# Optimization experiments

Measured on AMD Instinct MI355X. Metric: run time of the kernel, lower is better.

## Reference

```python
import jax, jax.numpy as jnp
import numpy as np

B, H, W, C = 2, 64, 64, 192
DM = int(2.0 * C)   # d_inner = ssm_ratio * hidden_dim = 384
N = 16              # d_state
R = 12              # dt_rank = ceil(C / 16)
K = 4               # scan directions


def _ln(x, g, b, eps):
    mu = jnp.mean(x, axis=-1, keepdims=True)
    var = jnp.var(x, axis=-1, keepdims=True)
    return (x - mu) * jax.lax.rsqrt(var + eps) * g + b


def setup_inputs() -> dict:
    key = jax.random.key(0)
    ks = jax.random.split(key, 8)
    return {
        "input": jax.random.normal(ks[0], (B, H, W, C), jnp.float32),
        "norm_g": jnp.ones((C,), jnp.float32),
        "norm_b": jnp.zeros((C,), jnp.float32),
        "in_proj_w": jax.random.normal(ks[1], (C, 2 * DM), jnp.float32) * 0.02,
        "conv_w": jax.random.normal(ks[2], (DM, 1, 3, 3), jnp.float32) * 0.1,
        "conv_b": jnp.zeros((DM,), jnp.float32),
        "x_proj_w": jax.random.normal(ks[3], (K, R + 2 * N, DM), jnp.float32) * 0.02,
        "dt_w": jax.random.normal(ks[4], (K, DM, R), jnp.float32) * 0.1,
        "dt_b": jax.random.uniform(ks[5], (K, DM), jnp.float32, -4.0, -2.0),
        "A_logs": jnp.tile(jnp.log(jnp.arange(1, N + 1, dtype=jnp.float32))[None, None, :], (K, DM, 1)),
        "Ds": jnp.ones((K, DM), jnp.float32),
        "out_norm_g": jnp.ones((DM,), jnp.float32),
        "out_norm_b": jnp.zeros((DM,), jnp.float32),
        "out_proj_w": jax.random.normal(ks[6], (DM, C), jnp.float32) * 0.02,
    }


def _selective_scan(us, deltas, A, Bs, Cs):
    # us, deltas: (B,K,D,L); A: (K,D,N); Bs, Cs: (B,K,N,L)
    u_l = jnp.moveaxis(us, -1, 0)       # (L,B,K,D)
    d_l = jnp.moveaxis(deltas, -1, 0)   # (L,B,K,D)
    B_l = jnp.moveaxis(Bs, -1, 0)       # (L,B,K,N)
    C_l = jnp.moveaxis(Cs, -1, 0)       # (L,B,K,N)
    h0 = jnp.zeros(us.shape[:3] + (A.shape[-1],), us.dtype)  # (B,K,D,N)

    def step(h, xs):
        u_t, d_t, b_t, c_t = xs
        dA = jnp.exp(d_t[..., None] * A)                       # (B,K,D,N)
        h = dA * h + (d_t * u_t)[..., None] * b_t[:, :, None, :]
        y = jnp.einsum('bkdn,bkn->bkd', h, c_t)
        return h, y

    _, ys = jax.lax.scan(step, h0, (u_l, d_l, B_l, C_l))
    return jnp.moveaxis(ys, 0, -1)  # (B,K,D,L)


def reference(input, norm_g, norm_b, in_proj_w, conv_w, conv_b, x_proj_w,
              dt_w, dt_b, A_logs, Ds, out_norm_g, out_norm_b, out_proj_w):
    Bz, Hh, Ww, Cc = input.shape
    L = Hh * Ww
    # pre-norm
    xn = _ln(input, norm_g, norm_b, 1e-6)
    # input projection -> x, z
    xz = xn @ in_proj_w                      # (B,H,W,2*DM)
    x, z = jnp.split(xz, 2, axis=-1)
    # depthwise conv + SiLU (channels-first)
    x = jnp.transpose(x, (0, 3, 1, 2))       # (B,DM,H,W)
    Dm = x.shape[1]
    x = jax.lax.conv_general_dilated(
        x, conv_w, (1, 1), 'SAME',
        dimension_numbers=('NCHW', 'OIHW', 'NCHW'),
        feature_group_count=Dm) + conv_b[None, :, None, None]
    x = jax.nn.silu(x)
    # 4-direction cross-scan: hw, wh, and their reverses
    x_flat = x.reshape(Bz, Dm, L)
    x_t = jnp.transpose(x, (0, 1, 3, 2)).reshape(Bz, Dm, L)
    xs = jnp.stack([x_flat, x_t], axis=1)                  # (B,2,DM,L)
    xs = jnp.concatenate([xs, jnp.flip(xs, -1)], axis=1)   # (B,4,DM,L)
    Rr = dt_w.shape[2]
    Nn = A_logs.shape[2]
    x_dbl = jnp.einsum('bkdl,kcd->bkcl', xs, x_proj_w)     # (B,4,R+2N,L)
    dts, Bs, Cs = jnp.split(x_dbl, [Rr, Rr + Nn], axis=2)
    deltas = jax.nn.softplus(
        jnp.einsum('bkrl,kdr->bkdl', dts, dt_w) + dt_b[None, :, :, None])
    A = -jnp.exp(A_logs)                                   # (4,DM,N)
    out_y = _selective_scan(xs, deltas, A, Bs, Cs) + Ds[None, :, :, None] * xs
    # merge the 4 directions back
    inv = jnp.flip(out_y[:, 2:], -1)

    def wh(t):
        return jnp.transpose(t.reshape(Bz, Dm, Ww, Hh), (0, 1, 3, 2)).reshape(Bz, Dm, L)

    y = out_y[:, 0] + inv[:, 0] + wh(out_y[:, 1]) + wh(inv[:, 1])  # (B,DM,L)
    y = jnp.transpose(y, (0, 2, 1))                                # (B,L,DM)
    y = _ln(y, out_norm_g, out_norm_b, 1e-5).reshape(Bz, Hh, Ww, Dm)
    y = y * jax.nn.silu(z)
    out = y @ out_proj_w
    # residual (drop_path=0 -> identity)
    return input + out
```

## Files before the change

kernel.cpp:

```cpp
#include <hip/hip_runtime.h>
#include <hip/hip_bf16.h>


typedef __attribute__((ext_vector_type(8))) short short8;
typedef __attribute__((ext_vector_type(4))) float floatx4;

__global__ __launch_bounds__(256) void k_ln(const float* __restrict__ in,
                                            const float* __restrict__ g,
                                            const float* __restrict__ be,
                                            __hip_bfloat16* __restrict__ out) {
  int row = blockIdx.x * 4 + (threadIdx.x >> 6);
  int lane = threadIdx.x & 63;
  const float* x = in + (long)row * 192;
  float v0 = x[lane], v1 = x[lane + 64], v2 = x[lane + 128];
  float s = v0 + v1 + v2;
  float s2 = v0 * v0 + v1 * v1 + v2 * v2;
  #pragma unroll
  for (int o = 32; o > 0; o >>= 1) { s += __shfl_xor(s, o); s2 += __shfl_xor(s2, o); }
  float mu = s * (1.f / 192.f);
  float var = s2 * (1.f / 192.f) - mu * mu;
  float r = rsqrtf(var + 1e-6f);
  __hip_bfloat16* op = out + (long)row * 192;
  op[lane]       = __float2bfloat16((v0 - mu) * r * g[lane]       + be[lane]);
  op[lane + 64]  = __float2bfloat16((v1 - mu) * r * g[lane + 64]  + be[lane + 64]);
  op[lane + 128] = __float2bfloat16((v2 - mu) * r * g[lane + 128] + be[lane + 128]);
}

__global__ __launch_bounds__(256) void k_packw(const float* __restrict__ ipw,
                                               const float* __restrict__ xpw,
                                               const float* __restrict__ opw,
                                               __hip_bfloat16* __restrict__ Wt1,
                                               __hip_bfloat16* __restrict__ Wt2,
                                               __hip_bfloat16* __restrict__ Wt3) {
  int idx = blockIdx.x * 256 + threadIdx.x;
  if (idx < 147456) {
    int n = idx / 192, k = idx - n * 192;
    Wt1[idx] = __float2bfloat16(ipw[(long)k * 768 + n]);
  } else if (idx < 147456 + 73728) {
    int t = idx - 147456;
    int j = t / 384;
    float v = (j < 176) ? xpw[t] : 0.f;
    Wt2[t] = __float2bfloat16(v);
  } else if (idx < 147456 + 73728 + 73728) {
    int t = idx - 147456 - 73728;
    int n = t / 384, k = t - n * 384;
    Wt3[t] = __float2bfloat16(opw[(long)k * 192 + n]);
  }
}

__device__ __forceinline__ int inv_dir(int k, int p) {
  int pt = ((p & 63) << 6) | (p >> 6);
  if (k == 0) return p;
  if (k == 1) return pt;
  if (k == 2) return 4095 - p;
  return 4095 - pt;
}
__device__ __forceinline__ int dir_pix(int k, int l) { return inv_dir(k, l); }

template <int EPI>
__global__ __launch_bounds__(256) void k_gemm_mfma(const __hip_bfloat16* __restrict__ A,
                                                   const __hip_bfloat16* __restrict__ Bt,
                                                   const float* __restrict__ Res,
                                                   float* __restrict__ Co,
                                                   __hip_bfloat16* __restrict__ CoB,
                                                   __hip_bfloat16* __restrict__ Co2B,
                                                   float* __restrict__ dtsS,
                                                   float* __restrict__ BsS,
                                                   float* __restrict__ CsS,
                                                   int M, int N, int Kk) {
  __shared__ __align__(16) short As[64 * 64];
  __shared__ __align__(16) short Bs[64 * 64];
  int tid = threadIdx.x;
  int wave = tid >> 6, lane = tid & 63;
  int mlane = lane & 15, quad = lane >> 4;
  int row0 = blockIdx.y * 64, col0 = blockIdx.x * 64;
  int wr = wave & 1, wc = wave >> 1;
  floatx4 acc[2][2];
  #pragma unroll
  for (int mi = 0; mi < 2; mi++)
    #pragma unroll
    for (int ni = 0; ni < 2; ni++) acc[mi][ni] = (floatx4){0.f, 0.f, 0.f, 0.f};

  for (int k0 = 0; k0 < Kk; k0 += 64) {
    #pragma unroll
    for (int c = tid; c < 512; c += 256) {
      int r = c >> 3, j = c & 7;
      *(float4*)&As[r * 64 + ((j ^ (r & 7)) << 3)] =
          *(const float4*)&A[(long)(row0 + r) * Kk + k0 + j * 8];
    }
    #pragma unroll
    for (int c = tid; c < 512; c += 256) {
      int r = c >> 3, j = c & 7;
      *(float4*)&Bs[r * 64 + ((j ^ (r & 7)) << 3)] =
          *(const float4*)&Bt[(long)(col0 + r) * Kk + k0 + j * 8];
    }
    __syncthreads();
    short8 af[2][2], bf[2][2];
    #pragma unroll
    for (int mi = 0; mi < 2; mi++) {
      int r = wr * 32 + mi * 16 + mlane;
      #pragma unroll
      for (int kk = 0; kk < 2; kk++) {
        int jx = (kk * 4 + quad) ^ (r & 7);
        af[mi][kk] = *(const short8*)&As[r * 64 + jx * 8];
      }
    }
    #pragma unroll
    for (int ni = 0; ni < 2; ni++) {
      int rn = wc * 32 + ni * 16 + mlane;
      #pragma unroll
      for (int kk = 0; kk < 2; kk++) {
        int jx = (kk * 4 + quad) ^ (rn & 7);
        bf[ni][kk] = *(const short8*)&Bs[rn * 64 + jx * 8];
      }
    }
    #pragma unroll
    for (int kk = 0; kk < 2; kk++)
      #pragma unroll
      for (int mi = 0; mi < 2; mi++)
        #pragma unroll
        for (int ni = 0; ni < 2; ni++)
          acc[mi][ni] = __builtin_amdgcn_mfma_f32_16x16x32_bf16(af[mi][kk], bf[ni][kk],
                                                                acc[mi][ni], 0, 0, 0);
    __syncthreads();
  }
  #pragma unroll
  for (int mi = 0; mi < 2; mi++) {
    #pragma unroll
    for (int ni = 0; ni < 2; ni++) {
      int cc = col0 + wc * 32 + ni * 16 + mlane;
      #pragma unroll
      for (int i = 0; i < 4; i++) {
        int rr = row0 + wr * 32 + mi * 16 + quad * 4 + i;
        float v = acc[mi][ni][i];
        if (EPI == 1) {
          Co[(long)rr * N + cc] = v + Res[(long)rr * N + cc];
        } else if (EPI == 2) {
          if (cc < 384) CoB[(long)rr * 384 + cc] = __float2bfloat16(v);
          else          Co2B[(long)rr * 384 + (cc - 384)] = __float2bfloat16(v);
        } else {
          if (cc < 176) {
            int k4 = (cc >= 132) ? 3 : (cc >= 88) ? 2 : (cc >= 44) ? 1 : 0;
            int c = cc - k4 * 44;
            int b = rr >> 12, p = rr & 4095;
            long lbase = ((long)((b << 2) + k4) << 12) + p;
            if (c < 12)      dtsS[lbase * 12 + c] = v;
            else if (c < 28) BsS[lbase * 16 + (c - 12)] = v;
            else             CsS[lbase * 16 + (c - 28)] = v;
          }
        }
      }
    }
  }
}

__global__ __launch_bounds__(384) void k_conv(const __hip_bfloat16* __restrict__ xbufB,
                                              const float* __restrict__ cw,
                                              const float* __restrict__ cb,
                                              __hip_bfloat16* __restrict__ xcb) {
  int row = blockIdx.x;
  int b = row >> 12, p = row & 4095;
  int h = p >> 6, w0 = p & 63;
  int d = threadIdx.x;
  float acc = cb[d];
  const float* wt = cw + d * 9;
  #pragma unroll
  for (int dh = -1; dh <= 1; dh++) {
    int hh = h + dh;
    if (hh < 0 || hh > 63) continue;
    #pragma unroll
    for (int dw = -1; dw <= 1; dw++) {
      int ww = w0 + dw;
      if (ww < 0 || ww > 63) continue;
      acc += __bfloat162float(xbufB[((long)(b << 12) + (hh << 6) + ww) * 384 + d])
             * wt[(dh + 1) * 3 + (dw + 1)];
    }
  }
  float sg = 1.f / (1.f + __expf(-acc));
  xcb[(long)row * 384 + d] = __float2bfloat16(acc * sg);
}

__device__ __forceinline__ void pow16(float r, float* pws) {
  pws[0] = r;
  #pragma unroll
  for (int n = 1; n < 16; n++) {
    int m = n + 1, c = (m + 1) / 2, f = m - c;
    pws[n] = pws[c - 1] * pws[f - 1];
  }
}

__global__ __launch_bounds__(384) void k_scan0(
    const float* __restrict__ dtsS, const float* __restrict__ BsS,
    const __hip_bfloat16* __restrict__ xcb,
    const float* __restrict__ A_logs, const float* __restrict__ dt_w,
    const float* __restrict__ dt_b,
    float* __restrict__ Eb, float* __restrict__ Dend) {
  int bid = blockIdx.x;
  int s = bid & 127, bk = bid >> 7;
  int k = bk & 3, b = bk >> 2;
  int d = threadIdx.x;
  float w[12];
  const float* dwp = dt_w + ((long)(k * 384) + d) * 12;
  #pragma unroll
  for (int r = 0; r < 12; r++) w[r] = dwp[r];
  float db = dt_b[k * 384 + d];
  const float* al = A_logs + ((long)(k * 384) + d) * 16;
  bool pw = true;
  float av[16];
  #pragma unroll
  for (int n = 0; n < 16; n++) {
    float a = __expf(al[n]);
    av[n] = -a;
    pw = pw && (fabsf(a - (float)(n + 1)) < 1e-3f);
  }
  float h[16];
  #pragma unroll
  for (int n = 0; n < 16; n++) h[n] = 0.f;
  float cum = 0.f;
  long bpk = (long)bk << 12;
  long bpix = (long)(b << 12);

  if (pw) {
    #pragma unroll 4
    for (int t = 0; t < 32; t++) {
      int p = dir_pix(k, s * 32 + t);
      const float4* dq = (const float4*)(dtsS + (bpk + p) * 12);
      float4 q0 = dq[0], q1 = dq[1], q2 = dq[2];
      float x = db + q0.x * w[0] + q0.y * w[1] + q0.z * w[2] + q0.w * w[3]
                   + q1.x * w[4] + q1.y * w[5] + q1.z * w[6] + q1.w * w[7]
                   + q2.x * w[8] + q2.y * w[9] + q2.z * w[10] + q2.w * w[11];
      float e = __expf(x);
      float delta = (x > 15.f) ? x : __logf(1.f + e);
      cum += delta;
      float u = __bfloat162float(xcb[(bpix + p) * 384 + d]);
      float du = delta * u;
      float rr = __builtin_amdgcn_rcpf(1.f + e);
      float pws[16]; pow16(rr, pws);
      const float4* Bq = (const float4*)(BsS + (bpk + p) * 16);
      float4 b0 = Bq[0], b1 = Bq[1], b2 = Bq[2], b3 = Bq[3];
      float Bl[16] = {b0.x, b0.y, b0.z, b0.w, b1.x, b1.y, b1.z, b1.w,
                      b2.x, b2.y, b2.z, b2.w, b3.x, b3.y, b3.z, b3.w};
      #pragma unroll
      for (int n = 0; n < 16; n++) h[n] = pws[n] * h[n] + du * Bl[n];
    }
  } else {
    for (int t = 0; t < 32; t++) {
      int p = dir_pix(k, s * 32 + t);
      const float4* dq = (const float4*)(dtsS + (bpk + p) * 12);
      float4 q0 = dq[0], q1 = dq[1], q2 = dq[2];
      float x = db + q0.x * w[0] + q0.y * w[1] + q0.z * w[2] + q0.w * w[3]
                   + q1.x * w[4] + q1.y * w[5] + q1.z * w[6] + q1.w * w[7]
                   + q2.x * w[8] + q2.y * w[9] + q2.z * w[10] + q2.w * w[11];
      float e = __expf(x);
      float delta = (x > 15.f) ? x : __logf(1.f + e);
      cum += delta;
      float u = __bfloat162float(xcb[(bpix + p) * 384 + d]);
      float du = delta * u;
      const float4* Bq = (const float4*)(BsS + (bpk + p) * 16);
      float4 b0 = Bq[0], b1 = Bq[1], b2 = Bq[2], b3 = Bq[3];
      float Bl[16] = {b0.x, b0.y, b0.z, b0.w, b1.x, b1.y, b1.z, b1.w,
                      b2.x, b2.y, b2.z, b2.w, b3.x, b3.y, b3.z, b3.w};
      #pragma unroll
      for (int n = 0; n < 16; n++) {
        float dA = __expf(delta * av[n]);
        h[n] = dA * h[n] + du * Bl[n];
      }
    }
  }
  long g = (long)bk * 128 + s;
  float* Ep = Eb + g * 6144 + d * 16;
  #pragma unroll
  for (int n = 0; n < 16; n++) Ep[n] = h[n];
  Dend[g * 384 + d] = cum;
}

__global__ __launch_bounds__(128) void k_combine(float* __restrict__ Eb,
                                                 const float* __restrict__ Dend,
                                                 const float* __restrict__ A_logs) {
  int bid = blockIdx.x;
  int bk = bid / 384;
  int d = bid - bk * 384;
  int k = bk & 3;
  int s = threadIdx.x;
  const float* al = A_logs + ((long)(k * 384) + d) * 16;
  float av[16];
  #pragma unroll
  for (int n = 0; n < 16; n++) av[n] = -__expf(al[n]);

  long ebase = ((long)bk * 128 + s) * 6144 + d * 16;
  float e[16];
  *(float4*)&e[0]  = *(const float4*)&Eb[ebase + 0];
  *(float4*)&e[4]  = *(const float4*)&Eb[ebase + 4];
  *(float4*)&e[8]  = *(const float4*)&Eb[ebase + 8];
  *(float4*)&e[12] = *(const float4*)&Eb[ebase + 12];
  float sig = Dend[((long)bk * 128 + s) * 384 + d];

  __shared__ float sE[128][17];
  sE[s][0] = sig;
  #pragma unroll
  for (int n = 0; n < 16; n++) sE[s][1 + n] = e[n];
  __syncthreads();

  for (int o = 1; o < 128; o <<= 1) {
    float ps = 0.f, pe[16];
    bool act = (s >= o);
    if (act) {
      ps = sE[s - o][0];
      #pragma unroll
      for (int n = 0; n < 16; n++) pe[n] = sE[s - o][1 + n];
    }
    __syncthreads();
    if (act) {
      #pragma unroll
      for (int n = 0; n < 16; n++) e[n] += __expf(av[n] * sig) * pe[n];
      sig += ps;
      sE[s][0] = sig;
      #pragma unroll
      for (int n = 0; n < 16; n++) sE[s][1 + n] = e[n];
    }
    __syncthreads();
  }

  float ho[16];
  if (s == 0) {
    #pragma unroll
    for (int n = 0; n < 16; n++) ho[n] = 0.f;
  } else {
    #pragma unroll
    for (int n = 0; n < 16; n++) ho[n] = sE[s - 1][1 + n];
  }
  *(float4*)&Eb[ebase + 0]  = *(float4*)&ho[0];
  *(float4*)&Eb[ebase + 4]  = *(float4*)&ho[4];
  *(float4*)&Eb[ebase + 8]  = *(float4*)&ho[8];
  *(float4*)&Eb[ebase + 12] = *(float4*)&ho[12];
}

template <int ATOMIC>
__global__ __launch_bounds__(384) void k_scan1(
    const float* __restrict__ dtsS, const float* __restrict__ BsS,
    const float* __restrict__ CsS, const __hip_bfloat16* __restrict__ xcb,
    const float* __restrict__ A_logs, const float* __restrict__ dt_w,
    const float* __restrict__ dt_b, const float* __restrict__ Eb,
    float* __restrict__ yout) {
  int bid = blockIdx.x;
  int s = bid & 127, bk = bid >> 7;
  int k = bk & 3, b = bk >> 2;
  int d = threadIdx.x;
  float w[12];
  const float* dwp = dt_w + ((long)(k * 384) + d) * 12;
  #pragma unroll
  for (int r = 0; r < 12; r++) w[r] = dwp[r];
  float db = dt_b[k * 384 + d];
  const float* al = A_logs + ((long)(k * 384) + d) * 16;
  bool pw = true;
  float av[16];
  #pragma unroll
  for (int n = 0; n < 16; n++) {
    float a = __expf(al[n]);
    av[n] = -a;
    pw = pw && (fabsf(a - (float)(n + 1)) < 1e-3f);
  }
  float h[16];
  const float* hp = Eb + ((long)bk * 128 + s) * 6144 + d * 16;
  #pragma unroll
  for (int n = 0; n < 16; n++) h[n] = hp[n];
  long bpk = (long)bk << 12;
  long bpix = (long)(b << 12);

  if (pw) {
    #pragma unroll 4
    for (int t = 0; t < 32; t++) {
      int p = dir_pix(k, s * 32 + t);
      const float4* dq = (const float4*)(dtsS + (bpk + p) * 12);
      float4 q0 = dq[0], q1 = dq[1], q2 = dq[2];
      float x = db + q0.x * w[0] + q0.y * w[1] + q0.z * w[2] + q0.w * w[3]
                   + q1.x * w[4] + q1.y * w[5] + q1.z * w[6] + q1.w * w[7]
                   + q2.x * w[8] + q2.y * w[9] + q2.z * w[10] + q2.w * w[11];
      float e = __expf(x);
      float delta = (x > 15.f) ? x : __logf(1.f + e);
      float u = __bfloat162float(xcb[(bpix + p) * 384 + d]);
      float du = delta * u;
      float rr = __builtin_amdgcn_rcpf(1.f + e);
      float pws[16]; pow16(rr, pws);
      const float4* Bq = (const float4*)(BsS + (bpk + p) * 16);
      float4 b0 = Bq[0], b1 = Bq[1], b2 = Bq[2], b3 = Bq[3];
      float Bl[16] = {b0.x, b0.y, b0.z, b0.w, b1.x, b1.y, b1.z, b1.w,
                      b2.x, b2.y, b2.z, b2.w, b3.x, b3.y, b3.z, b3.w};
      const float4* Cq = (const float4*)(CsS + (bpk + p) * 16);
      float4 c0 = Cq[0], c1 = Cq[1], c2 = Cq[2], c3 = Cq[3];
      float Cl[16] = {c0.x, c0.y, c0.z, c0.w, c1.x, c1.y, c1.z, c1.w,
                      c2.x, c2.y, c2.z, c2.w, c3.x, c3.y, c3.z, c3.w};
      float y = 0.f;
      #pragma unroll
      for (int n = 0; n < 16; n++) { h[n] = pws[n] * h[n] + du * Bl[n]; y += h[n] * Cl[n]; }
      if (ATOMIC) atomicAdd(&yout[(bpix + p) * 384 + d], y);
      else        yout[(bpk + p) * 384 + d] = y;
    }
  } else {
    for (int t = 0; t < 32; t++) {
      int p = dir_pix(k, s * 32 + t);
      const float4* dq = (const float4*)(dtsS + (bpk + p) * 12);
      float4 q0 = dq[0], q1 = dq[1], q2 = dq[2];
      float x = db + q0.x * w[0] + q0.y * w[1] + q0.z * w[2] + q0.w * w[3]
                   + q1.x * w[4] + q1.y * w[5] + q1.z * w[6] + q1.w * w[7]
                   + q2.x * w[8] + q2.y * w[9] + q2.z * w[10] + q2.w * w[11];
      float e = __expf(x);
      float delta = (x > 15.f) ? x : __logf(1.f + e);
      float u = __bfloat162float(xcb[(bpix + p) * 384 + d]);
      float du = delta * u;
      const float4* Bq = (const float4*)(BsS + (bpk + p) * 16);
      float4 b0 = Bq[0], b1 = Bq[1], b2 = Bq[2], b3 = Bq[3];
      float Bl[16] = {b0.x, b0.y, b0.z, b0.w, b1.x, b1.y, b1.z, b1.w,
                      b2.x, b2.y, b2.z, b2.w, b3.x, b3.y, b3.z, b3.w};
      const float4* Cq = (const float4*)(CsS + (bpk + p) * 16);
      float4 c0 = Cq[0], c1 = Cq[1], c2 = Cq[2], c3 = Cq[3];
      float Cl[16] = {c0.x, c0.y, c0.z, c0.w, c1.x, c1.y, c1.z, c1.w,
                      c2.x, c2.y, c2.z, c2.w, c3.x, c3.y, c3.z, c3.w};
      float y = 0.f;
      #pragma unroll
      for (int n = 0; n < 16; n++) {
        float dA = __expf(delta * av[n]);
        h[n] = dA * h[n] + du * Bl[n];
        y += h[n] * Cl[n];
      }
      if (ATOMIC) atomicAdd(&yout[(bpix + p) * 384 + d], y);
      else        yout[(bpk + p) * 384 + d] = y;
    }
  }
}

template <int GATHER>
__global__ __launch_bounds__(384) void k_merge(const float* __restrict__ yin,
                                               const __hip_bfloat16* __restrict__ xcb,
                                               const __hip_bfloat16* __restrict__ zbufB,
                                               const float* __restrict__ Ds,
                                               const float* __restrict__ g,
                                               const float* __restrict__ be,
                                               __hip_bfloat16* __restrict__ yactb) {
  int row = blockIdx.x;
  int d = threadIdx.x;
  float v;
  if (GATHER) {
    int b = row >> 12, p = row & 4095;
    long base = ((long)(b << 2) << 12) + p;
    v = yin[base * 384 + d]
      + yin[(base + 4096) * 384 + d]
      + yin[(base + 8192) * 384 + d]
      + yin[(base + 12288) * 384 + d];
  } else {
    v = yin[(long)row * 384 + d];
  }
  float sd = Ds[d] + Ds[384 + d] + Ds[768 + d] + Ds[1152 + d];
  v += __bfloat162float(xcb[(long)row * 384 + d]) * sd;
  float s1 = v, s2 = v * v;
  #pragma unroll
  for (int o = 32; o > 0; o >>= 1) { s1 += __shfl_xor(s1, o); s2 += __shfl_xor(s2, o); }
  __shared__ float r1[6], r2[6];
  int wv = threadIdx.x >> 6;
  if ((threadIdx.x & 63) == 0) { r1[wv] = s1; r2[wv] = s2; }
  __syncthreads();
  float S1 = 0.f, S2 = 0.f;
  #pragma unroll
  for (int i = 0; i < 6; i++) { S1 += r1[i]; S2 += r2[i]; }
  float mu = S1 * (1.f / 384.f);
  float var = S2 * (1.f / 384.f) - mu * mu;
  float rr = rsqrtf(var + 1e-5f);
  float yn = (v - mu) * rr * g[d] + be[d];
  float z = __bfloat162float(zbufB[(long)row * 384 + d]);
  float sg = z / (1.f + __expf(-z));
  yactb[(long)row * 384 + d] = __float2bfloat16(yn * sg);
}

extern "C" void kernel_launch(void* const* d_in, const int* in_sizes, int n_in,
                              void* d_out, int out_size, void* d_ws, size_t ws_size,
                              hipStream_t stream) {
  const float* input      = (const float*)d_in[0];
  const float* norm_g     = (const float*)d_in[1];
  const float* norm_b     = (const float*)d_in[2];
  const float* in_proj_w  = (const float*)d_in[3];
  const float* conv_w     = (const float*)d_in[4];
  const float* conv_b     = (const float*)d_in[5];
  const float* x_proj_w   = (const float*)d_in[6];
  const float* dt_w       = (const float*)d_in[7];
  const float* dt_b       = (const float*)d_in[8];
  const float* A_logs     = (const float*)d_in[9];
  const float* Ds         = (const float*)d_in[10];
  const float* out_norm_g = (const float*)d_in[11];
  const float* out_norm_b = (const float*)d_in[12];
  const float* out_proj_w = (const float*)d_in[13];
  float* out = (float*)d_out;

  float* ws = (float*)d_ws;
  long o = 0;
  __hip_bfloat16* xnb   = (__hip_bfloat16*)(ws + o); o += 786432;
  __hip_bfloat16* xbufB = (__hip_bfloat16*)(ws + o); o += 1572864;
  __hip_bfloat16* zbufB = (__hip_bfloat16*)(ws + o); o += 1572864;
  __hip_bfloat16* xcb   = (__hip_bfloat16*)(ws + o); o += 1572864;
  __hip_bfloat16* Wt1   = (__hip_bfloat16*)(ws + o); o += 73728;
  __hip_bfloat16* Wt2   = (__hip_bfloat16*)(ws + o); o += 36864;
  __hip_bfloat16* Wt3   = (__hip_bfloat16*)(ws + o); o += 36864;
  float* dtsS           = ws + o;                    o += 393216;
  float* BsS            = ws + o;                    o += 524288;
  float* CsS            = ws + o;                    o += 524288;
  float* Eb             = ws + o;                    o += 6291456;
  float* Dend           = ws + o;                    o += 393216;
  bool big = ws_size >= (size_t)27934720 * 4;
  float* ybuf           = ws + o;                    o += big ? 12582912 : 3145728;
  __hip_bfloat16* yactb = (__hip_bfloat16*)(ws + o); o += 1572864;

  k_ln<<<dim3(2048), dim3(256), 0, stream>>>(input, norm_g, norm_b, xnb);
  k_packw<<<dim3(1152), dim3(256), 0, stream>>>(in_proj_w, x_proj_w, out_proj_w, Wt1, Wt2, Wt3);
  k_gemm_mfma<2><<<dim3(12, 128), dim3(256), 0, stream>>>(xnb, Wt1, nullptr, nullptr, xbufB, zbufB,
                                                          nullptr, nullptr, nullptr, 8192, 768, 192);
  k_conv<<<dim3(8192), dim3(384), 0, stream>>>(xbufB, conv_w, conv_b, xcb);
  k_gemm_mfma<3><<<dim3(3, 128), dim3(256), 0, stream>>>(xcb, Wt2, nullptr, nullptr, nullptr, nullptr,
                                                         dtsS, BsS, CsS, 8192, 192, 384);
  k_scan0<<<dim3(1024), dim3(384), 0, stream>>>(dtsS, BsS, xcb, A_logs, dt_w, dt_b, Eb, Dend);
  k_combine<<<dim3(3072), dim3(128), 0, stream>>>(Eb, Dend, A_logs);
  if (big) {
    k_scan1<0><<<dim3(1024), dim3(384), 0, stream>>>(dtsS, BsS, CsS, xcb, A_logs, dt_w, dt_b, Eb, ybuf);
    k_merge<1><<<dim3(8192), dim3(384), 0, stream>>>(ybuf, xcb, zbufB, Ds, out_norm_g, out_norm_b, yactb);
  } else {
    hipMemsetAsync(ybuf, 0, (size_t)3145728 * 4, stream);
    k_scan1<1><<<dim3(1024), dim3(384), 0, stream>>>(dtsS, BsS, CsS, xcb, A_logs, dt_w, dt_b, Eb, ybuf);
    k_merge<0><<<dim3(8192), dim3(384), 0, stream>>>(ybuf, xcb, zbufB, Ds, out_norm_g, out_norm_b, yactb);
  }
  k_gemm_mfma<1><<<dim3(3, 128), dim3(256), 0, stream>>>(yactb, Wt3, input, out, nullptr, nullptr,
                                                         nullptr, nullptr, nullptr, 8192, 192, 384);
}
```

Baseline: 264.8 us.

## Stage scan chunk dt/B/C in LDS, prefetch u, use power trick in combine

Each scan block now cooperatively loads its chunk's dt, B and C rows into shared memory once, instead of every thread issuing redundant uniform global loads per timestep. The per-element u value is software-prefetched one step ahead to hide global latency. The combine kernel also uses the integer-A power shortcut (one exp plus multiplies) in place of 16 exps when A matches 1..N. The cost is extra LDS, a barrier, and one wasted prefetch at the end of each chunk.

```diff
diff --git a/kernel.cpp b/kernel.cpp
--- a/kernel.cpp
+++ b/kernel.cpp
@@ -195,10 +195,24 @@
     const float* __restrict__ A_logs, const float* __restrict__ dt_w,
     const float* __restrict__ dt_b,
     float* __restrict__ Eb, float* __restrict__ Dend) {
+  __shared__ __align__(16) float sD[384];
+  __shared__ __align__(16) float sB[512];
   int bid = blockIdx.x;
   int s = bid & 127, bk = bid >> 7;
   int k = bk & 3, b = bk >> 2;
   int d = threadIdx.x;
+  long bpk = (long)bk << 12;
+  long bpix = (long)(b << 12);
+  {
+    int t = d / 12, r = d - t * 12;
+    sD[d] = dtsS[(bpk + dir_pix(k, s * 32 + t)) * 12 + r];
+    int t2 = d >> 4, r2 = d & 15;
+    sB[d] = BsS[(bpk + dir_pix(k, s * 32 + t2)) * 16 + r2];
+    if (d < 128) {
+      int t3 = 24 + (d >> 4);
+      sB[384 + d] = BsS[(bpk + dir_pix(k, s * 32 + t3)) * 16 + (d & 15)];
+    }
+  }
   float w[12];
   const float* dwp = dt_w + ((long)(k * 384) + d) * 12;
   #pragma unroll
@@ -217,14 +231,17 @@
   #pragma unroll
   for (int n = 0; n < 16; n++) h[n] = 0.f;
   float cum = 0.f;
-  long bpk = (long)bk << 12;
-  long bpix = (long)(b << 12);
+  __syncthreads();
+
+  float u_nxt = __bfloat162float(xcb[(bpix + dir_pix(k, s * 32)) * 384 + d]);
 
   if (pw) {
     #pragma unroll 4
     for (int t = 0; t < 32; t++) {
-      int p = dir_pix(k, s * 32 + t);
-      const float4* dq = (const float4*)(dtsS + (bpk + p) * 12);
+      float u = u_nxt;
+      int pn = dir_pix(k, s * 32 + ((t + 1) & 31));
+      u_nxt = __bfloat162float(xcb[(bpix + pn) * 384 + d]);
+      const float4* dq = (const float4*)&sD[t * 12];
       float4 q0 = dq[0], q1 = dq[1], q2 = dq[2];
       float x = db + q0.x * w[0] + q0.y * w[1] + q0.z * w[2] + q0.w * w[3]
                    + q1.x * w[4] + q1.y * w[5] + q1.z * w[6] + q1.w * w[7]
@@ -232,11 +249,10 @@
       float e = __expf(x);
       float delta = (x > 15.f) ? x : __logf(1.f + e);
       cum += delta;
-      float u = __bfloat162float(xcb[(bpix + p) * 384 + d]);
       float du = delta * u;
       float rr = __builtin_amdgcn_rcpf(1.f + e);
       float pws[16]; pow16(rr, pws);
-      const float4* Bq = (const float4*)(BsS + (bpk + p) * 16);
+      const float4* Bq = (const float4*)&sB[t * 16];
       float4 b0 = Bq[0], b1 = Bq[1], b2 = Bq[2], b3 = Bq[3];
       float Bl[16] = {b0.x, b0.y, b0.z, b0.w, b1.x, b1.y, b1.z, b1.w,
                       b2.x, b2.y, b2.z, b2.w, b3.x, b3.y, b3.z, b3.w};
@@ -245,8 +261,10 @@
     }
   } else {
     for (int t = 0; t < 32; t++) {
-      int p = dir_pix(k, s * 32 + t);
-      const float4* dq = (const float4*)(dtsS + (bpk + p) * 12);
+      float u = u_nxt;
+      int pn = dir_pix(k, s * 32 + ((t + 1) & 31));
+      u_nxt = __bfloat162float(xcb[(bpix + pn) * 384 + d]);
+      const float4* dq = (const float4*)&sD[t * 12];
       float4 q0 = dq[0], q1 = dq[1], q2 = dq[2];
       float x = db + q0.x * w[0] + q0.y * w[1] + q0.z * w[2] + q0.w * w[3]
                    + q1.x * w[4] + q1.y * w[5] + q1.z * w[6] + q1.w * w[7]
@@ -254,9 +272,8 @@
       float e = __expf(x);
       float delta = (x > 15.f) ? x : __logf(1.f + e);
       cum += delta;
-      float u = __bfloat162float(xcb[(bpix + p) * 384 + d]);
       float du = delta * u;
-      const float4* Bq = (const float4*)(BsS + (bpk + p) * 16);
+      const float4* Bq = (const float4*)&sB[t * 16];
       float4 b0 = Bq[0], b1 = Bq[1], b2 = Bq[2], b3 = Bq[3];
       float Bl[16] = {b0.x, b0.y, b0.z, b0.w, b1.x, b1.y, b1.z, b1.w,
                       b2.x, b2.y, b2.z, b2.w, b3.x, b3.y, b3.z, b3.w};
@@ -283,9 +300,14 @@
   int k = bk & 3;
   int s = threadIdx.x;
   const float* al = A_logs + ((long)(k * 384) + d) * 16;
+  bool pw = true;
   float av[16];
   #pragma unroll
-  for (int n = 0; n < 16; n++) av[n] = -__expf(al[n]);
+  for (int n = 0; n < 16; n++) {
+    float a = __expf(al[n]);
+    av[n] = -a;
+    pw = pw && (fabsf(a - (float)(n + 1)) < 1e-3f);
+  }
 
   long ebase = ((long)bk * 128 + s) * 6144 + d * 16;
   float e[16];
@@ -311,8 +333,15 @@
     }
     __syncthreads();
     if (act) {
-      #pragma unroll
-      for (int n = 0; n < 16; n++) e[n] += __expf(av[n] * sig) * pe[n];
+      if (pw) {
+        float rc = __expf(-sig);
+        float pwr[16]; pow16(rc, pwr);
+        #pragma unroll
+        for (int n = 0; n < 16; n++) e[n] += pwr[n] * pe[n];
+      } else {
+        #pragma unroll
+        for (int n = 0; n < 16; n++) e[n] += __expf(av[n] * sig) * pe[n];
+      }
       sig += ps;
       sE[s][0] = sig;
       #pragma unroll
@@ -342,10 +371,29 @@
     const float* __restrict__ A_logs, const float* __restrict__ dt_w,
     const float* __restrict__ dt_b, const float* __restrict__ Eb,
     float* __restrict__ yout) {
+  __shared__ __align__(16) float sD[384];
+  __shared__ __align__(16) float sB[512];
+  __shared__ __align__(16) float sC[512];
   int bid = blockIdx.x;
   int s = bid & 127, bk = bid >> 7;
   int k = bk & 3, b = bk >> 2;
   int d = threadIdx.x;
+  long bpk = (long)bk << 12;
+  long bpix = (long)(b << 12);
+  {
+    int t = d / 12, r = d - t * 12;
+    sD[d] = dtsS[(bpk + dir_pix(k, s * 32 + t)) * 12 + r];
+    int t2 = d >> 4, r2 = d & 15;
+    int p2 = dir_pix(k, s * 32 + t2);
+    sB[d] = BsS[(bpk + p2) * 16 + r2];
+    sC[d] = CsS[(bpk + p2) * 16 + r2];
+    if (d < 128) {
+      int t3 = 24 + (d >> 4);
+      int p3 = dir_pix(k, s * 32 + t3);
+      sB[384 + d] = BsS[(bpk + p3) * 16 + (d & 15)];
+      sC[384 + d] = CsS[(bpk + p3) * 16 + (d & 15)];
+    }
+  }
   float w[12];
   const float* dwp = dt_w + ((long)(k * 384) + d) * 12;
   #pragma unroll
@@ -364,29 +412,33 @@
   const float* hp = Eb + ((long)bk * 128 + s) * 6144 + d * 16;
   #pragma unroll
   for (int n = 0; n < 16; n++) h[n] = hp[n];
-  long bpk = (long)bk << 12;
-  long bpix = (long)(b << 12);
+  __syncthreads();
+
+  int pc = dir_pix(k, s * 32);
+  float u_nxt = __bfloat162float(xcb[(bpix + pc) * 384 + d]);
 
   if (pw) {
     #pragma unroll 4
     for (int t = 0; t < 32; t++) {
-      int p = dir_pix(k, s * 32 + t);
-      const float4* dq = (const float4*)(dtsS + (bpk + p) * 12);
+      int p = pc;
+      float u = u_nxt;
+      pc = dir_pix(k, s * 32 + ((t + 1) & 31));
+      u_nxt = __bfloat162float(xcb[(bpix + pc) * 384 + d]);
+      const float4* dq = (const float4*)&sD[t * 12];
       float4 q0 = dq[0], q1 = dq[1], q2 = dq[2];
       float x = db + q0.x * w[0] + q0.y * w[1] + q0.z * w[2] + q0.w * w[3]
                    + q1.x * w[4] + q1.y * w[5] + q1.z * w[6] + q1.w * w[7]
                    + q2.x * w[8] + q2.y * w[9] + q2.z * w[10] + q2.w * w[11];
       float e = __expf(x);
       float delta = (x > 15.f) ? x : __logf(1.f + e);
-      float u = __bfloat162float(xcb[(bpix + p) * 384 + d]);
       float du = delta * u;
       float rr = __builtin_amdgcn_rcpf(1.f + e);
       float pws[16]; pow16(rr, pws);
-      const float4* Bq = (const float4*)(BsS + (bpk + p) * 16);
+      const float4* Bq = (const float4*)&sB[t * 16];
       float4 b0 = Bq[0], b1 = Bq[1], b2 = Bq[2], b3 = Bq[3];
       float Bl[16] = {b0.x, b0.y, b0.z, b0.w, b1.x, b1.y, b1.z, b1.w,
                       b2.x, b2.y, b2.z, b2.w, b3.x, b3.y, b3.z, b3.w};
-      const float4* Cq = (const float4*)(CsS + (bpk + p) * 16);
+      const float4* Cq = (const float4*)&sC[t * 16];
       float4 c0 = Cq[0], c1 = Cq[1], c2 = Cq[2], c3 = Cq[3];
       float Cl[16] = {c0.x, c0.y, c0.z, c0.w, c1.x, c1.y, c1.z, c1.w,
                       c2.x, c2.y, c2.z, c2.w, c3.x, c3.y, c3.z, c3.w};
@@ -398,21 +450,23 @@
     }
   } else {
     for (int t = 0; t < 32; t++) {
-      int p = dir_pix(k, s * 32 + t);
-      const float4* dq = (const float4*)(dtsS + (bpk + p) * 12);
+      int p = pc;
+      float u = u_nxt;
+      pc = dir_pix(k, s * 32 + ((t + 1) & 31));
+      u_nxt = __bfloat162float(xcb[(bpix + pc) * 384 + d]);
+      const float4* dq = (const float4*)&sD[t * 12];
       float4 q0 = dq[0], q1 = dq[1], q2 = dq[2];
       float x = db + q0.x * w[0] + q0.y * w[1] + q0.z * w[2] + q0.w * w[3]
                    + q1.x * w[4] + q1.y * w[5] + q1.z * w[6] + q1.w * w[7]
                    + q2.x * w[8] + q2.y * w[9] + q2.z * w[10] + q2.w * w[11];
       float e = __expf(x);
       float delta = (x > 15.f) ? x : __logf(1.f + e);
-      float u = __bfloat162float(xcb[(bpix + p) * 384 + d]);
-      float du = delta * u;
-      const float4* Bq = (const float4*)(BsS + (bpk + p) * 16);
+      float u2 = delta * u;
+      const float4* Bq = (const float4*)&sB[t * 16];
       float4 b0 = Bq[0], b1 = Bq[1], b2 = Bq[2], b3 = Bq[3];
       float Bl[16] = {b0.x, b0.y, b0.z, b0.w, b1.x, b1.y, b1.z, b1.w,
                       b2.x, b2.y, b2.z, b2.w, b3.x, b3.y, b3.z, b3.w};
-      const float4* Cq = (const float4*)(CsS + (bpk + p) * 16);
+      const float4* Cq = (const float4*)&sC[t * 16];
       float4 c0 = Cq[0], c1 = Cq[1], c2 = Cq[2], c3 = Cq[3];
       float Cl[16] = {c0.x, c0.y, c0.z, c0.w, c1.x, c1.y, c1.z, c1.w,
                       c2.x, c2.y, c2.z, c2.w, c3.x, c3.y, c3.z, c3.w};
@@ -420,7 +474,7 @@
       #pragma unroll
       for (int n = 0; n < 16; n++) {
         float dA = __expf(delta * av[n]);
-        h[n] = dA * h[n] + du * Bl[n];
+        h[n] = dA * h[n] + u2 * Bl[n];
         y += h[n] * Cl[n];
       }
       if (ATOMIC) atomicAdd(&yout[(bpix + p) * 384 + d], y);
```

New measurement: 277.1 us. 4.6% more time.

## Split selective scan into shorter chunks and use power trick in combine

Applied to the files above, without the earlier changes.

The chunked scan is templated on chunk length T, and when the workspace is large enough it uses 16-step chunks (256 segments) instead of 32, doubling the grid of the two scan passes. The combine kernel is templated on segment count and gains a fast path that replaces 16 exponentials with one exp plus repeated multiplication when A follows the default integer pattern. This shortens the serial per-thread work and adds parallelism, at the cost of a longer inter-segment prefix combine and more carry-state traffic in Eb.

```diff
diff --git a/kernel.cpp b/kernel.cpp
--- a/kernel.cpp
+++ b/kernel.cpp
@@ -189,14 +189,16 @@
   }
 }
 
+template <int T>
 __global__ __launch_bounds__(384) void k_scan0(
     const float* __restrict__ dtsS, const float* __restrict__ BsS,
     const __hip_bfloat16* __restrict__ xcb,
     const float* __restrict__ A_logs, const float* __restrict__ dt_w,
     const float* __restrict__ dt_b,
     float* __restrict__ Eb, float* __restrict__ Dend) {
+  constexpr int SEG = 4096 / T;
   int bid = blockIdx.x;
-  int s = bid & 127, bk = bid >> 7;
+  int s = bid & (SEG - 1), bk = bid / SEG;
   int k = bk & 3, b = bk >> 2;
   int d = threadIdx.x;
   float w[12];
@@ -222,8 +224,8 @@
 
   if (pw) {
     #pragma unroll 4
-    for (int t = 0; t < 32; t++) {
-      int p = dir_pix(k, s * 32 + t);
+    for (int t = 0; t < T; t++) {
+      int p = dir_pix(k, s * T + t);
       const float4* dq = (const float4*)(dtsS + (bpk + p) * 12);
       float4 q0 = dq[0], q1 = dq[1], q2 = dq[2];
       float x = db + q0.x * w[0] + q0.y * w[1] + q0.z * w[2] + q0.w * w[3]
@@ -244,8 +246,8 @@
       for (int n = 0; n < 16; n++) h[n] = pws[n] * h[n] + du * Bl[n];
     }
   } else {
-    for (int t = 0; t < 32; t++) {
-      int p = dir_pix(k, s * 32 + t);
+    for (int t = 0; t < T; t++) {
+      int p = dir_pix(k, s * T + t);
       const float4* dq = (const float4*)(dtsS + (bpk + p) * 12);
       float4 q0 = dq[0], q1 = dq[1], q2 = dq[2];
       float x = db + q0.x * w[0] + q0.y * w[1] + q0.z * w[2] + q0.w * w[3]
@@ -267,14 +269,15 @@
       }
     }
   }
-  long g = (long)bk * 128 + s;
+  long g = (long)bk * SEG + s;
   float* Ep = Eb + g * 6144 + d * 16;
   #pragma unroll
   for (int n = 0; n < 16; n++) Ep[n] = h[n];
   Dend[g * 384 + d] = cum;
 }
 
-__global__ __launch_bounds__(128) void k_combine(float* __restrict__ Eb,
+template <int SEG>
+__global__ __launch_bounds__(SEG) void k_combine(float* __restrict__ Eb,
                                                  const float* __restrict__ Dend,
                                                  const float* __restrict__ A_logs) {
   int bid = blockIdx.x;
@@ -283,25 +286,30 @@
   int k = bk & 3;
   int s = threadIdx.x;
   const float* al = A_logs + ((long)(k * 384) + d) * 16;
+  bool pw = true;
   float av[16];
   #pragma unroll
-  for (int n = 0; n < 16; n++) av[n] = -__expf(al[n]);
-
-  long ebase = ((long)bk * 128 + s) * 6144 + d * 16;
+  for (int n = 0; n < 16; n++) {
+    float a = __expf(al[n]);
+    av[n] = -a;
+    pw = pw && (fabsf(a - (float)(n + 1)) < 1e-3f);
+  }
+
+  long ebase = ((long)bk * SEG + s) * 6144 + d * 16;
   float e[16];
   *(float4*)&e[0]  = *(const float4*)&Eb[ebase + 0];
   *(float4*)&e[4]  = *(const float4*)&Eb[ebase + 4];
   *(float4*)&e[8]  = *(const float4*)&Eb[ebase + 8];
   *(float4*)&e[12] = *(const float4*)&Eb[ebase + 12];
-  float sig = Dend[((long)bk * 128 + s) * 384 + d];
-
-  __shared__ float sE[128][17];
+  float sig = Dend[((long)bk * SEG + s) * 384 + d];
+
+  __shared__ float sE[SEG][17];
   sE[s][0] = sig;
   #pragma unroll
   for (int n = 0; n < 16; n++) sE[s][1 + n] = e[n];
   __syncthreads();
 
-  for (int o = 1; o < 128; o <<= 1) {
+  for (int o = 1; o < SEG; o <<= 1) {
     float ps = 0.f, pe[16];
     bool act = (s >= o);
     if (act) {
@@ -311,8 +319,15 @@
     }
     __syncthreads();
     if (act) {
-      #pragma unroll
-      for (int n = 0; n < 16; n++) e[n] += __expf(av[n] * sig) * pe[n];
+      if (pw) {
+        float rc = __expf(-sig);
+        float pwr[16]; pow16(rc, pwr);
+        #pragma unroll
+        for (int n = 0; n < 16; n++) e[n] += pwr[n] * pe[n];
+      } else {
+        #pragma unroll
+        for (int n = 0; n < 16; n++) e[n] += __expf(av[n] * sig) * pe[n];
+      }
       sig += ps;
       sE[s][0] = sig;
       #pragma unroll
@@ -335,15 +350,16 @@
   *(float4*)&Eb[ebase + 12] = *(float4*)&ho[12];
 }
 
-template <int ATOMIC>
+template <int T, int ATOMIC>
 __global__ __launch_bounds__(384) void k_scan1(
     const float* __restrict__ dtsS, const float* __restrict__ BsS,
     const float* __restrict__ CsS, const __hip_bfloat16* __restrict__ xcb,
     const float* __restrict__ A_logs, const float* __restrict__ dt_w,
     const float* __restrict__ dt_b, const float* __restrict__ Eb,
     float* __restrict__ yout) {
+  constexpr int SEG = 4096 / T;
   int bid = blockIdx.x;
-  int s = bid & 127, bk = bid >> 7;
+  int s = bid & (SEG - 1), bk = bid / SEG;
   int k = bk & 3, b = bk >> 2;
   int d = threadIdx.x;
   float w[12];
@@ -361,7 +377,7 @@
     pw = pw && (fabsf(a - (float)(n + 1)) < 1e-3f);
   }
   float h[16];
-  const float* hp = Eb + ((long)bk * 128 + s) * 6144 + d * 16;
+  const float* hp = Eb + ((long)bk * SEG + s) * 6144 + d * 16;
   #pragma unroll
   for (int n = 0; n < 16; n++) h[n] = hp[n];
   long bpk = (long)bk << 12;
@@ -369,8 +385,8 @@
 
   if (pw) {
     #pragma unroll 4
-    for (int t = 0; t < 32; t++) {
-      int p = dir_pix(k, s * 32 + t);
+    for (int t = 0; t < T; t++) {
+      int p = dir_pix(k, s * T + t);
       const float4* dq = (const float4*)(dtsS + (bpk + p) * 12);
       float4 q0 = dq[0], q1 = dq[1], q2 = dq[2];
       float x = db + q0.x * w[0] + q0.y * w[1] + q0.z * w[2] + q0.w * w[3]
@@ -397,8 +413,8 @@
       else        yout[(bpk + p) * 384 + d] = y;
     }
   } else {
-    for (int t = 0; t < 32; t++) {
-      int p = dir_pix(k, s * 32 + t);
+    for (int t = 0; t < T; t++) {
+      int p = dir_pix(k, s * T + t);
       const float4* dq = (const float4*)(dtsS + (bpk + p) * 12);
       float4 q0 = dq[0], q1 = dq[1], q2 = dq[2];
       float x = db + q0.x * w[0] + q0.y * w[1] + q0.z * w[2] + q0.w * w[3]
@@ -490,6 +506,10 @@
   const float* out_proj_w = (const float*)d_in[13];
   float* out = (float*)d_out;
 
+  bool big2 = ws_size >= (size_t)34619392 * 4;
+  bool big  = ws_size >= (size_t)27934720 * 4;
+  int SEG = big2 ? 256 : 128;
+
   float* ws = (float*)d_ws;
   long o = 0;
   __hip_bfloat16* xnb   = (__hip_bfloat16*)(ws + o); o += 786432;
@@ -502,9 +522,8 @@
   float* dtsS           = ws + o;                    o += 393216;
   float* BsS            = ws + o;                    o += 524288;
   float* CsS            = ws + o;                    o += 524288;
-  float* Eb             = ws + o;                    o += 6291456;
-  float* Dend           = ws + o;                    o += 393216;
-  bool big = ws_size >= (size_t)27934720 * 4;
+  float* Eb             = ws + o;                    o += (long)8 * SEG * 6144;
+  float* Dend           = ws + o;                    o += (long)8 * SEG * 384;
   float* ybuf           = ws + o;                    o += big ? 12582912 : 3145728;
   __hip_bfloat16* yactb = (__hip_bfloat16*)(ws + o); o += 1572864;
 
@@ -515,14 +534,21 @@
   k_conv<<<dim3(8192), dim3(384), 0, stream>>>(xbufB, conv_w, conv_b, xcb);
   k_gemm_mfma<3><<<dim3(3, 128), dim3(256), 0, stream>>>(xcb, Wt2, nullptr, nullptr, nullptr, nullptr,
                                                          dtsS, BsS, CsS, 8192, 192, 384);
-  k_scan0<<<dim3(1024), dim3(384), 0, stream>>>(dtsS, BsS, xcb, A_logs, dt_w, dt_b, Eb, Dend);
-  k_combine<<<dim3(3072), dim3(128), 0, stream>>>(Eb, Dend, A_logs);
-  if (big) {
-    k_scan1<0><<<dim3(1024), dim3(384), 0, stream>>>(dtsS, BsS, CsS, xcb, A_logs, dt_w, dt_b, Eb, ybuf);
+  if (big2) {
+    k_scan0<16><<<dim3(2048), dim3(384), 0, stream>>>(dtsS, BsS, xcb, A_logs, dt_w, dt_b, Eb, Dend);
+    k_combine<256><<<dim3(3072), dim3(256), 0, stream>>>(Eb, Dend, A_logs);
+    k_scan1<16, 0><<<dim3(2048), dim3(384), 0, stream>>>(dtsS, BsS, CsS, xcb, A_logs, dt_w, dt_b, Eb, ybuf);
+    k_merge<1><<<dim3(8192), dim3(384), 0, stream>>>(ybuf, xcb, zbufB, Ds, out_norm_g, out_norm_b, yactb);
+  } else if (big) {
+    k_scan0<32><<<dim3(1024), dim3(384), 0, stream>>>(dtsS, BsS, xcb, A_logs, dt_w, dt_b, Eb, Dend);
+    k_combine<128><<<dim3(3072), dim3(128), 0, stream>>>(Eb, Dend, A_logs);
+    k_scan1<32, 0><<<dim3(1024), dim3(384), 0, stream>>>(dtsS, BsS, CsS, xcb, A_logs, dt_w, dt_b, Eb, ybuf);
     k_merge<1><<<dim3(8192), dim3(384), 0, stream>>>(ybuf, xcb, zbufB, Ds, out_norm_g, out_norm_b, yactb);
   } else {
+    k_scan0<32><<<dim3(1024), dim3(384), 0, stream>>>(dtsS, BsS, xcb, A_logs, dt_w, dt_b, Eb, Dend);
+    k_combine<128><<<dim3(3072), dim3(128), 0, stream>>>(Eb, Dend, A_logs);
     hipMemsetAsync(ybuf, 0, (size_t)3145728 * 4, stream);
-    k_scan1<1><<<dim3(1024), dim3(384), 0, stream>>>(dtsS, BsS, CsS, xcb, A_logs, dt_w, dt_b, Eb, ybuf);
+    k_scan1<32, 1><<<dim3(1024), dim3(384), 0, stream>>>(dtsS, BsS, CsS, xcb, A_logs, dt_w, dt_b, Eb, ybuf);
     k_merge<0><<<dim3(8192), dim3(384), 0, stream>>>(ybuf, xcb, zbufB, Ds, out_norm_g, out_norm_b, yactb);
   }
   k_gemm_mfma<1><<<dim3(3, 128), dim3(256), 0, stream>>>(yactb, Wt3, input, out, nullptr, nullptr,
```

After: 290.6 us. 1.1x slower.

## Precompute softplus deltas in fp16 once and reuse across both scan passes

Applied to the files above, without the earlier changes.

Adds a k_dt kernel that computes delta = softplus(dt_w·dts + dt_b) once per (b,k,l,d) and stores it as fp16. Both scan passes then load it instead of recomputing the 12-term dot product and exp/log, and the power-of-two decay base becomes exp(-delta). k_combine also gets the pow16 fast path for integer A, replacing 16 exps per step with one. The trade is an extra 12.6 MB write and two reads of that buffer, which may cost more than the arithmetic it saves. Storing delta in fp16 also loses precision, and the larger workspace requirement may switch execution to the atomic fallback path.

```diff
diff --git a/kernel.cpp b/kernel.cpp
--- a/kernel.cpp
+++ b/kernel.cpp
@@ -1,5 +1,6 @@
 #include <hip/hip_runtime.h>
 #include <hip/hip_bf16.h>
+#include <hip/hip_fp16.h>
 
 
 typedef __attribute__((ext_vector_type(8))) short short8;
@@ -180,6 +181,33 @@
   xcb[(long)row * 384 + d] = __float2bfloat16(acc * sg);
 }
 
+__global__ __launch_bounds__(384) void k_dt(const float* __restrict__ dtsS,
+                                            const float* __restrict__ dt_w,
+                                            const float* __restrict__ dt_b,
+                                            __half* __restrict__ dpre) {
+  int bid = blockIdx.x;
+  int chunk = bid & 127, bk = bid >> 7;
+  int k = bk & 3;
+  int d = threadIdx.x;
+  float w[12];
+  const float* dwp = dt_w + ((long)(k * 384) + d) * 12;
+  #pragma unroll
+  for (int r = 0; r < 12; r++) w[r] = dwp[r];
+  float db = dt_b[k * 384 + d];
+  long base = ((long)bk << 12) + chunk * 32;
+  #pragma unroll 4
+  for (int t = 0; t < 32; t++) {
+    const float4* dq = (const float4*)(dtsS + (base + t) * 12);
+    float4 q0 = dq[0], q1 = dq[1], q2 = dq[2];
+    float x = db + q0.x * w[0] + q0.y * w[1] + q0.z * w[2] + q0.w * w[3]
+                 + q1.x * w[4] + q1.y * w[5] + q1.z * w[6] + q1.w * w[7]
+                 + q2.x * w[8] + q2.y * w[9] + q2.z * w[10] + q2.w * w[11];
+    float e = __expf(x);
+    float delta = (x > 15.f) ? x : __logf(1.f + e);
+    dpre[(base + t) * 384 + d] = __float2half(delta);
+  }
+}
+
 __device__ __forceinline__ void pow16(float r, float* pws) {
   pws[0] = r;
   #pragma unroll
@@ -190,20 +218,14 @@
 }
 
 __global__ __launch_bounds__(384) void k_scan0(
-    const float* __restrict__ dtsS, const float* __restrict__ BsS,
+    const __half* __restrict__ dpre, const float* __restrict__ BsS,
     const __hip_bfloat16* __restrict__ xcb,
-    const float* __restrict__ A_logs, const float* __restrict__ dt_w,
-    const float* __restrict__ dt_b,
+    const float* __restrict__ A_logs,
     float* __restrict__ Eb, float* __restrict__ Dend) {
   int bid = blockIdx.x;
   int s = bid & 127, bk = bid >> 7;
   int k = bk & 3, b = bk >> 2;
   int d = threadIdx.x;
-  float w[12];
-  const float* dwp = dt_w + ((long)(k * 384) + d) * 12;
-  #pragma unroll
-  for (int r = 0; r < 12; r++) w[r] = dwp[r];
-  float db = dt_b[k * 384 + d];
   const float* al = A_logs + ((long)(k * 384) + d) * 16;
   bool pw = true;
   float av[16];
@@ -224,17 +246,11 @@
     #pragma unroll 4
     for (int t = 0; t < 32; t++) {
       int p = dir_pix(k, s * 32 + t);
-      const float4* dq = (const float4*)(dtsS + (bpk + p) * 12);
-      float4 q0 = dq[0], q1 = dq[1], q2 = dq[2];
-      float x = db + q0.x * w[0] + q0.y * w[1] + q0.z * w[2] + q0.w * w[3]
-                   + q1.x * w[4] + q1.y * w[5] + q1.z * w[6] + q1.w * w[7]
-                   + q2.x * w[8] + q2.y * w[9] + q2.z * w[10] + q2.w * w[11];
-      float e = __expf(x);
-      float delta = (x > 15.f) ? x : __logf(1.f + e);
+      float delta = __half2float(dpre[(bpk + p) * 384 + d]);
       cum += delta;
       float u = __bfloat162float(xcb[(bpix + p) * 384 + d]);
       float du = delta * u;
-      float rr = __builtin_amdgcn_rcpf(1.f + e);
+      float rr = __expf(-delta);
       float pws[16]; pow16(rr, pws);
       const float4* Bq = (const float4*)(BsS + (bpk + p) * 16);
       float4 b0 = Bq[0], b1 = Bq[1], b2 = Bq[2], b3 = Bq[3];
@@ -246,13 +262,7 @@
   } else {
     for (int t = 0; t < 32; t++) {
       int p = dir_pix(k, s * 32 + t);
-      const float4* dq = (const float4*)(dtsS + (bpk + p) * 12);
-      float4 q0 = dq[0], q1 = dq[1], q2 = dq[2];
-      float x = db + q0.x * w[0] + q0.y * w[1] + q0.z * w[2] + q0.w * w[3]
-                   + q1.x * w[4] + q1.y * w[5] + q1.z * w[6] + q1.w * w[7]
-                   + q2.x * w[8] + q2.y * w[9] + q2.z * w[10] + q2.w * w[11];
-      float e = __expf(x);
-      float delta = (x > 15.f) ? x : __logf(1.f + e);
+      float delta = __half2float(dpre[(bpk + p) * 384 + d]);
       cum += delta;
       float u = __bfloat162float(xcb[(bpix + p) * 384 + d]);
       float du = delta * u;
@@ -283,9 +293,14 @@
   int k = bk & 3;
   int s = threadIdx.x;
   const float* al = A_logs + ((long)(k * 384) + d) * 16;
+  bool pw = true;
   float av[16];
   #pragma unroll
-  for (int n = 0; n < 16; n++) av[n] = -__expf(al[n]);
+  for (int n = 0; n < 16; n++) {
+    float a = __expf(al[n]);
+    av[n] = -a;
+    pw = pw && (fabsf(a - (float)(n + 1)) < 1e-3f);
+  }
 
   long ebase = ((long)bk * 128 + s) * 6144 + d * 16;
   float e[16];
@@ -311,8 +326,15 @@
     }
     __syncthreads();
     if (act) {
-      #pragma unroll
-      for (int n = 0; n < 16; n++) e[n] += __expf(av[n] * sig) * pe[n];
+      if (pw) {
+        float rc = __expf(-sig);
+        float pwr[16]; pow16(rc, pwr);
+        #pragma unroll
+        for (int n = 0; n < 16; n++) e[n] += pwr[n] * pe[n];
+      } else {
+        #pragma unroll
+        for (int n = 0; n < 16; n++) e[n] += __expf(av[n] * sig) * pe[n];
+      }
       sig += ps;
       sE[s][0] = sig;
       #pragma unroll
@@ -337,20 +359,14 @@
 
 template <int ATOMIC>
 __global__ __launch_bounds__(384) void k_scan1(
-    const float* __restrict__ dtsS, const float* __restrict__ BsS,
+    const __half* __restrict__ dpre, const float* __restrict__ BsS,
     const float* __restrict__ CsS, const __hip_bfloat16* __restrict__ xcb,
-    const float* __restrict__ A_logs, const float* __restrict__ dt_w,
-    const float* __restrict__ dt_b, const float* __restrict__ Eb,
+    const float* __restrict__ A_logs, const float* __restrict__ Eb,
     float* __restrict__ yout) {
   int bid = blockIdx.x;
   int s = bid & 127, bk = bid >> 7;
   int k = bk & 3, b = bk >> 2;
   int d = threadIdx.x;
-  float w[12];
-  const float* dwp = dt_w + ((long)(k * 384) + d) * 12;
-  #pragma unroll
-  for (int r = 0; r < 12; r++) w[r] = dwp[r];
-  float db = dt_b[k * 384 + d];
   const float* al = A_logs + ((long)(k * 384) + d) * 16;
   bool pw = true;
   float av[16];
@@ -371,16 +387,10 @@
     #pragma unroll 4
     for (int t = 0; t < 32; t++) {
       int p = dir_pix(k, s * 32 + t);
-      const float4* dq = (const float4*)(dtsS + (bpk + p) * 12);
-      float4 q0 = dq[0], q1 = dq[1], q2 = dq[2];
-      float x = db + q0.x * w[0] + q0.y * w[1] + q0.z * w[2] + q0.w * w[3]
-                   + q1.x * w[4] + q1.y * w[5] + q1.z * w[6] + q1.w * w[7]
-                   + q2.x * w[8] + q2.y * w[9] + q2.z * w[10] + q2.w * w[11];
-      float e = __expf(x);
-      float delta = (x > 15.f) ? x : __logf(1.f + e);
+      float delta = __half2float(dpre[(bpk + p) * 384 + d]);
       float u = __bfloat162float(xcb[(bpix + p) * 384 + d]);
       float du = delta * u;
-      float rr = __builtin_amdgcn_rcpf(1.f + e);
+      float rr = __expf(-delta);
       float pws[16]; pow16(rr, pws);
       const float4* Bq = (const float4*)(BsS + (bpk + p) * 16);
       float4 b0 = Bq[0], b1 = Bq[1], b2 = Bq[2], b3 = Bq[3];
@@ -399,13 +409,7 @@
   } else {
     for (int t = 0; t < 32; t++) {
       int p = dir_pix(k, s * 32 + t);
-      const float4* dq = (const float4*)(dtsS + (bpk + p) * 12);
-      float4 q0 = dq[0], q1 = dq[1], q2 = dq[2];
-      float x = db + q0.x * w[0] + q0.y * w[1] + q0.z * w[2] + q0.w * w[3]
-                   + q1.x * w[4] + q1.y * w[5] + q1.z * w[6] + q1.w * w[7]
-                   + q2.x * w[8] + q2.y * w[9] + q2.z * w[10] + q2.w * w[11];
-      float e = __expf(x);
-      float delta = (x > 15.f) ? x : __logf(1.f + e);
+      float delta = __half2float(dpre[(bpk + p) * 384 + d]);
       float u = __bfloat162float(xcb[(bpix + p) * 384 + d]);
       float du = delta * u;
       const float4* Bq = (const float4*)(BsS + (bpk + p) * 16);
@@ -490,6 +494,8 @@
   const float* out_proj_w = (const float*)d_in[13];
   float* out = (float*)d_out;
 
+  bool big = ws_size >= (size_t)34226176 * 4;
+
   float* ws = (float*)d_ws;
   long o = 0;
   __hip_bfloat16* xnb   = (__hip_bfloat16*)(ws + o); o += 786432;
@@ -502,9 +508,9 @@
   float* dtsS           = ws + o;                    o += 393216;
   float* BsS            = ws + o;                    o += 524288;
   float* CsS            = ws + o;                    o += 524288;
+  __half* dpre          = (__half*)(ws + o);         o += 6291456;
   float* Eb             = ws + o;                    o += 6291456;
   float* Dend           = ws + o;                    o += 393216;
-  bool big = ws_size >= (size_t)27934720 * 4;
   float* ybuf           = ws + o;                    o += big ? 12582912 : 3145728;
   __hip_bfloat16* yactb = (__hip_bfloat16*)(ws + o); o += 1572864;
 
@@ -515,14 +521,15 @@
   k_conv<<<dim3(8192), dim3(384), 0, stream>>>(xbufB, conv_w, conv_b, xcb);
   k_gemm_mfma<3><<<dim3(3, 128), dim3(256), 0, stream>>>(xcb, Wt2, nullptr, nullptr, nullptr, nullptr,
                                                          dtsS, BsS, CsS, 8192, 192, 384);
-  k_scan0<<<dim3(1024), dim3(384), 0, stream>>>(dtsS, BsS, xcb, A_logs, dt_w, dt_b, Eb, Dend);
+  k_dt<<<dim3(1024), dim3(384), 0, stream>>>(dtsS, dt_w, dt_b, dpre);
+  k_scan0<<<dim3(1024), dim3(384), 0, stream>>>(dpre, BsS, xcb, A_logs, Eb, Dend);
   k_combine<<<dim3(3072), dim3(128), 0, stream>>>(Eb, Dend, A_logs);
   if (big) {
-    k_scan1<0><<<dim3(1024), dim3(384), 0, stream>>>(dtsS, BsS, CsS, xcb, A_logs, dt_w, dt_b, Eb, ybuf);
+    k_scan1<0><<<dim3(1024), dim3(384), 0, stream>>>(dpre, BsS, CsS, xcb, A_logs, Eb, ybuf);
     k_merge<1><<<dim3(8192), dim3(384), 0, stream>>>(ybuf, xcb, zbufB, Ds, out_norm_g, out_norm_b, yactb);
   } else {
     hipMemsetAsync(ybuf, 0, (size_t)3145728 * 4, stream);
-    k_scan1<1><<<dim3(1024), dim3(384), 0, stream>>>(dtsS, BsS, CsS, xcb, A_logs, dt_w, dt_b, Eb, ybuf);
+    k_scan1<1><<<dim3(1024), dim3(384), 0, stream>>>(dpre, BsS, CsS, xcb, A_logs, Eb, ybuf);
     k_merge<0><<<dim3(8192), dim3(384), 0, stream>>>(ybuf, xcb, zbufB, Ds, out_norm_g, out_norm_b, yactb);
   }
   k_gemm_mfma<1><<<dim3(3, 128), dim3(256), 0, stream>>>(yactb, Wt3, input, out, nullptr, nullptr,
```

Measured after the change: 261.6 us. Within noise of the previous version (-1.2%).
